# Optimization experiments

Measured on AMD Instinct MI355X. Metric: run time of the kernel, lower is better.

The kernel has to match this reference:

```python
import math
import jax, jax.numpy as jnp
from jax import lax
import numpy as np

C_CURV = 0.01
CHUNK = 1024
EPS = 1e-15
TANH_CLIP = 1.0 - 1e-6


def safe_norm(x):
    return jnp.maximum(jnp.linalg.norm(x, axis=-1, keepdims=True), EPS)


def exp_map_zero(v, c):
    sqrt_c = math.sqrt(c)
    vn = safe_norm(v)
    return jnp.tanh(sqrt_c * vn) * v / (sqrt_c * vn)


def log_map_zero(y, c):
    sqrt_c = math.sqrt(c)
    yn = safe_norm(y)
    arg = jnp.clip(sqrt_c * yn, -TANH_CLIP, TANH_CLIP)
    return jnp.arctanh(arg) * y / (sqrt_c * yn)


def mobius_add(x, y, c):
    x2 = jnp.sum(x * x, axis=-1, keepdims=True)
    y2 = jnp.sum(y * y, axis=-1, keepdims=True)
    xy = jnp.sum(x * y, axis=-1, keepdims=True)
    num = (1.0 + 2.0 * c * xy + c * y2) * x + (1.0 - c * x2) * y
    den = 1.0 + 2.0 * c * xy + (c * c) * x2 * y2
    return num / jnp.maximum(den, EPS)


def givens_rotation(x, angles):
    # x: (B, d), angles: (B, d/2)
    x1 = x[:, 0::2]
    x2 = x[:, 1::2]
    cos_a = jnp.cos(angles)
    sin_a = jnp.sin(angles)
    out1 = cos_a * x1 - sin_a * x2
    out2 = sin_a * x1 + cos_a * x2
    # interleave back: stack on axis 2 then flatten
    return jnp.stack([out1, out2], axis=2).reshape(x.shape[0], x.shape[1])


def setup_inputs() -> dict:
    key = jax.random.key(0)
    k1, k2, k3, k4, k5, k6 = jax.random.split(key, 6)
    E, R, D, B = 40960, 480, 512, 128
    # keep entity points well inside the Poincare ball of curvature c
    entity_embedding = 0.05 * jax.random.normal(k1, (E, D), dtype=jnp.float32)
    rel_embedding = jax.random.normal(k2, (R, D), dtype=jnp.float32)  # unused, interface parity
    rel_rot = jax.random.uniform(k3, (R, D // 2), dtype=jnp.float32,
                                 minval=-math.pi, maxval=math.pi)
    rel_trans = jax.random.uniform(k4, (R, D), dtype=jnp.float32,
                                   minval=-0.001, maxval=0.001)
    entity_bias = jnp.zeros((E,), dtype=jnp.float32)
    triplets = jax.random.randint(k6, (B, 3), 0, R, dtype=jnp.int64)
    return {
        "entity_embedding": entity_embedding,
        "rel_embedding": rel_embedding,
        "rel_rot": rel_rot,
        "rel_trans": rel_trans,
        "entity_bias": entity_bias,
        "triplets": triplets,
    }


def reference(entity_embedding, rel_embedding, rel_rot, rel_trans, entity_bias, triplets):
    c = C_CURV
    E, D = entity_embedding.shape
    r_idx = triplets[:, 1]
    s_emb = entity_embedding[triplets[:, 0]]            # (B, d)
    s_tan = log_map_zero(s_emb, c)
    rot_s_tan = givens_rotation(s_tan, rel_rot[r_idx])
    rot_s = exp_map_zero(rot_s_tan, c)
    t_r = exp_map_zero(rel_trans[r_idx], c)
    query = mobius_add(rot_s, t_r, c)                   # (B, d)

    n_chunks = E // CHUNK
    ent_chunks = entity_embedding.reshape(n_chunks, CHUNK, D)
    bias_chunks = entity_bias.reshape(n_chunks, CHUNK)

    neg_q = -query[:, None, :]                          # (B, 1, d)

    def body(_, inp):
        cand, b = inp                                   # (CHUNK, d), (CHUNK,)
        diff = mobius_add(neg_q, cand[None, :, :], c)   # (B, CHUNK, d)
        dist_sq = jnp.sum(diff * diff, axis=-1)         # (B, CHUNK)
        return None, -dist_sq + b[None, :]

    _, chunks = lax.scan(body, None, (ent_chunks, bias_chunks))  # (n_chunks, B, CHUNK)
    scores = jnp.transpose(chunks, (1, 0, 2)).reshape(query.shape[0], E)
    scores = scores + entity_bias[triplets[:, 0]][:, None]
    return scores
```

## Files before the change

kernel.cpp:

```cpp
#include <hip/hip_runtime.h>
#include <math.h>

#define C_C   0.01f
#define SQC   0.1f
#define EPSF  1e-15f
#define TCLIP (1.0f - 1e-6f)

typedef short short8 __attribute__((ext_vector_type(8)));
typedef float f32x4  __attribute__((ext_vector_type(4)));

__device__ __forceinline__ float wred(float v) {
#pragma unroll
    for (int off = 32; off > 0; off >>= 1) v += __shfl_xor(v, off, 64);
    return v;
}

__device__ __forceinline__ float dot4(const float4& a, const float4& b) {
    return a.x * b.x + a.y * b.y + a.z * b.z + a.w * b.w;
}

__device__ __forceinline__ unsigned int f2bf(float f) {
    unsigned int u = __float_as_uint(f);
    u += 0x7fffu + ((u >> 16) & 1u);
    return u >> 16;
}
__device__ __forceinline__ unsigned int pk2(float a, float b) {
    return f2bf(a) | (f2bf(b) << 16);
}

__global__ __launch_bounds__(64)
void build_queries(const float* __restrict__ ent,
                   const float* __restrict__ rrot,
                   const float* __restrict__ rtrans,
                   const float* __restrict__ ebias,
                   const int* __restrict__ trip,
                   unsigned short* __restrict__ qb,
                   float* __restrict__ q2buf,
                   float* __restrict__ sbbuf)
{
    const int b    = blockIdx.x;
    const int lane = threadIdx.x;
    const int t0   = trip[b * 3 + 0];
    const int r    = trip[b * 3 + 1];

    const float* srow = ent + (size_t)t0 * 512;
    float4 s0 = *(const float4*)(srow + 4 * lane);
    float4 s1 = *(const float4*)(srow + 256 + 4 * lane);

    float ss = dot4(s0, s0) + dot4(s1, s1);
    ss = wred(ss);
    float yn  = fmaxf(sqrtf(ss), EPSF);
    float arg = fminf(SQC * yn, TCLIP);
    float fl  = atanhf(arg) / (SQC * yn);

    const float* arow = rrot + (size_t)r * 256;
    float2 a01 = *(const float2*)(arow + 2 * lane);
    float2 a23 = *(const float2*)(arow + 128 + 2 * lane);
    float c0, n0, c1, n1, c2, n2, c3, n3;
    sincosf(a01.x, &n0, &c0);
    sincosf(a01.y, &n1, &c1);
    sincosf(a23.x, &n2, &c2);
    sincosf(a23.y, &n3, &c3);

    float t0x = s0.x * fl, t0y = s0.y * fl, t0z = s0.z * fl, t0w = s0.w * fl;
    float t1x = s1.x * fl, t1y = s1.y * fl, t1z = s1.z * fl, t1w = s1.w * fl;

    float4 r0, r1;
    r0.x = c0 * t0x - n0 * t0y;  r0.y = n0 * t0x + c0 * t0y;
    r0.z = c1 * t0z - n1 * t0w;  r0.w = n1 * t0z + c1 * t0w;
    r1.x = c2 * t1x - n2 * t1y;  r1.y = n2 * t1x + c2 * t1y;
    r1.z = c3 * t1z - n3 * t1w;  r1.w = n3 * t1z + c3 * t1w;

    float vv = dot4(r0, r0) + dot4(r1, r1);
    vv = wred(vv);
    float vn = fmaxf(sqrtf(vv), EPSF);
    float fx = tanhf(SQC * vn) / (SQC * vn);

    const float* trow = rtrans + (size_t)r * 512;
    float4 u0 = *(const float4*)(trow + 4 * lane);
    float4 u1 = *(const float4*)(trow + 256 + 4 * lane);
    float tt = dot4(u0, u0) + dot4(u1, u1);
    float rt = dot4(r0, u0) + dot4(r1, u1);
    tt = wred(tt);
    rt = wred(rt);
    float tn = fmaxf(sqrtf(tt), EPSF);
    float fy = tanhf(SQC * tn) / (SQC * tn);

    float x2 = fx * fx * vv;
    float y2 = fy * fy * tt;
    float xy = fx * fy * rt;
    float ca  = 1.0f + 2.0f * C_C * xy + C_C * y2;
    float cb  = 1.0f - C_C * x2;
    float den = fmaxf(1.0f + 2.0f * C_C * xy + C_C * C_C * x2 * y2, EPSF);
    float inv = 1.0f / den;

    float4 q0, q1;
    q0.x = (ca * fx * r0.x + cb * fy * u0.x) * inv;
    q0.y = (ca * fx * r0.y + cb * fy * u0.y) * inv;
    q0.z = (ca * fx * r0.z + cb * fy * u0.z) * inv;
    q0.w = (ca * fx * r0.w + cb * fy * u0.w) * inv;
    q1.x = (ca * fx * r1.x + cb * fy * u1.x) * inv;
    q1.y = (ca * fx * r1.y + cb * fy * u1.y) * inv;
    q1.z = (ca * fx * r1.z + cb * fy * u1.z) * inv;
    q1.w = (ca * fx * r1.w + cb * fy * u1.w) * inv;

    float qq = dot4(q0, q0) + dot4(q1, q1);
    qq = wred(qq);

    unsigned short* qrow = qb + (size_t)b * 512;
    uint2 h0, h1;
    h0.x = pk2(q0.x, q0.y);  h0.y = pk2(q0.z, q0.w);
    h1.x = pk2(q1.x, q1.y);  h1.y = pk2(q1.z, q1.w);
    *(uint2*)(qrow + 4 * lane)       = h0;
    *(uint2*)(qrow + 256 + 4 * lane) = h1;
    if (lane == 0) {
        q2buf[b] = qq;
        sbbuf[b] = ebias[t0];
    }
}

__global__ __launch_bounds__(64, 4)
void score_direct(const float* __restrict__ ent,
                  const float* __restrict__ ebias,
                  const unsigned short* __restrict__ qb,
                  const float* __restrict__ q2buf,
                  const float* __restrict__ sbbuf,
                  float* __restrict__ out, int E)
{
    const int lane = threadIdx.x;
    const int er   = lane & 15;
    const int kg   = lane >> 4;
    const int e0   = blockIdx.x * 16;

    short8 eb[16];
    float  e2p = 0.0f;
    const float* esrc = ent + (size_t)(e0 + er) * 512 + kg * 8;
#pragma unroll
    for (int ks = 0; ks < 16; ++ks) {
        float4 f0 = *(const float4*)(esrc + ks * 32);
        float4 f1 = *(const float4*)(esrc + ks * 32 + 4);
        e2p += dot4(f0, f0) + dot4(f1, f1);
        uint4 p = { pk2(f0.x, f0.y), pk2(f0.z, f0.w),
                    pk2(f1.x, f1.y), pk2(f1.z, f1.w) };
        eb[ks] = *(short8*)&p;
    }
    e2p += __shfl_xor(e2p, 16, 64);
    e2p += __shfl_xor(e2p, 32, 64);
    const float e2 = e2p;
    const float be = ebias[e0 + er];

    for (int qg = 0; qg < 8; ++qg) {
        f32x4 acc = (f32x4)0.0f;
        const unsigned short* qp =
            qb + (size_t)(qg * 16 + er) * 512 + kg * 8;
#pragma unroll
        for (int ks = 0; ks < 16; ++ks) {
            short8 a = *(const short8*)(qp + ks * 32);
            acc = __builtin_amdgcn_mfma_f32_16x16x32_bf16(a, eb[ks], acc,
                                                          0, 0, 0);
        }
        float4 q2v = *(const float4*)(q2buf + qg * 16 + kg * 4);
        float4 sbv = *(const float4*)(sbbuf + qg * 16 + kg * 4);
        const float q2a[4] = { q2v.x, q2v.y, q2v.z, q2v.w };
        const float sba[4] = { sbv.x, sbv.y, sbv.z, sbv.w };
#pragma unroll
        for (int r = 0; r < 4; ++r) {
            const int q   = qg * 16 + kg * 4 + r;
            float q2  = q2a[r];
            float xy  = -acc[r];
            float ca  = 1.0f + 2.0f * C_C * xy + C_C * e2;
            float cb  = 1.0f - C_C * q2;
            float den = fmaxf(1.0f + 2.0f * C_C * xy + C_C * C_C * q2 * e2, EPSF);
            float id2 = 1.0f / (den * den);
            float dist = (ca * ca * q2 + 2.0f * ca * cb * xy + cb * cb * e2) * id2;
            out[(size_t)q * E + e0 + er] = sba[r] + be - dist;
        }
    }
}

extern "C" void kernel_launch(void* const* d_in, const int* in_sizes, int n_in,
                              void* d_out, int out_size, void* d_ws, size_t ws_size,
                              hipStream_t stream) {
    const float* ent    = (const float*)d_in[0];
    const float* rrot   = (const float*)d_in[2];
    const float* rtrans = (const float*)d_in[3];
    const float* ebias  = (const float*)d_in[4];
    const int*   trip   = (const int*)d_in[5];
    float* out = (float*)d_out;

    const int B = in_sizes[5] / 3;
    const int E = in_sizes[0] / 512;

    unsigned short* qb = (unsigned short*)d_ws;
    float* q2buf = (float*)(qb + (size_t)B * 512);
    float* sbbuf = q2buf + B;

    build_queries<<<B, 64, 0, stream>>>(ent, rrot, rtrans, ebias, trip,
                                        qb, q2buf, sbbuf);
    score_direct<<<E / 16, 64, 0, stream>>>(ent, ebias, qb, q2buf, sbbuf,
                                            out, E);
}
```

Before: 171.4 us.

## Split K dimension across four waves with LDS reduction in scoring kernel

The scoring kernel now uses 256-thread blocks where each of four wavefronts handles a 128-wide slice of the 512-dim reduction for the same 16 entities. Partial MFMA accumulators are reduced through shared memory in two steps, and each wave then finishes the distance epilogue for two query groups. It also software-prefetches the next query group's bf16 fragments while issuing MFMAs. This aims to expose more parallelism and cut the per-wave serial MFMA chain and register footprint, at the cost of LDS traffic and two block barriers.

New measurement: 170.1 us. No clear change (-0.8%).

```diff
diff --git a/kernel.cpp b/kernel.cpp
--- a/kernel.cpp
+++ b/kernel.cpp
@@ -119,26 +119,36 @@
     }
 }
 
-__global__ __launch_bounds__(64, 4)
-void score_direct(const float* __restrict__ ent,
+__global__ __launch_bounds__(256, 4)
+void score_ksplit(const float* __restrict__ ent,
                   const float* __restrict__ ebias,
                   const unsigned short* __restrict__ qb,
                   const float* __restrict__ q2buf,
                   const float* __restrict__ sbbuf,
                   float* __restrict__ out, int E)
 {
-    const int lane = threadIdx.x;
+    __shared__ float part[2][8][64][4];
+    __shared__ float e2part[4][16];
+
+    const int tid  = threadIdx.x;
+    const int lane = tid & 63;
+    const int w    = tid >> 6;
     const int er   = lane & 15;
     const int kg   = lane >> 4;
     const int e0   = blockIdx.x * 16;
-
-    short8 eb[16];
+    const int k0   = w * 128 + kg * 8;
+
+    const float* esrc = ent + (size_t)(e0 + er) * 512 + k0;
+    float4 f[8];
+#pragma unroll
+    for (int i = 0; i < 8; ++i)
+        f[i] = *(const float4*)(esrc + (i >> 1) * 32 + (i & 1) * 4);
+
+    short8 eb[4];
     float  e2p = 0.0f;
-    const float* esrc = ent + (size_t)(e0 + er) * 512 + kg * 8;
-#pragma unroll
-    for (int ks = 0; ks < 16; ++ks) {
-        float4 f0 = *(const float4*)(esrc + ks * 32);
-        float4 f1 = *(const float4*)(esrc + ks * 32 + 4);
+#pragma unroll
+    for (int ks = 0; ks < 4; ++ks) {
+        float4 f0 = f[2 * ks], f1 = f[2 * ks + 1];
         e2p += dot4(f0, f0) + dot4(f1, f1);
         uint4 p = { pk2(f0.x, f0.y), pk2(f0.z, f0.w),
                     pk2(f1.x, f1.y), pk2(f1.z, f1.w) };
@@ -146,28 +156,69 @@
     }
     e2p += __shfl_xor(e2p, 16, 64);
     e2p += __shfl_xor(e2p, 32, 64);
-    const float e2 = e2p;
+    if (lane < 16) e2part[w][er] = e2p;
+
+    const unsigned short* qbase = qb + (size_t)er * 512 + k0;
+    f32x4 acc[8];
+#pragma unroll
+    for (int qg = 0; qg < 8; ++qg) acc[qg] = (f32x4)0.0f;
+
+    short8 qa[4], qn[4];
+#pragma unroll
+    for (int ks = 0; ks < 4; ++ks)
+        qa[ks] = *(const short8*)(qbase + ks * 32);
+
+#pragma unroll
+    for (int qg = 0; qg < 8; ++qg) {
+        if (qg < 7) {
+#pragma unroll
+            for (int ks = 0; ks < 4; ++ks)
+                qn[ks] = *(const short8*)(qbase + (size_t)(qg + 1) * 16 * 512
+                                          + ks * 32);
+        }
+#pragma unroll
+        for (int ks = 0; ks < 4; ++ks)
+            acc[qg] = __builtin_amdgcn_mfma_f32_16x16x32_bf16(
+                qa[ks], eb[ks], acc[qg], 0, 0, 0);
+#pragma unroll
+        for (int ks = 0; ks < 4; ++ks) qa[ks] = qn[ks];
+    }
+
+    if (w < 2) {
+#pragma unroll
+        for (int qg = 0; qg < 8; ++qg)
+            *(f32x4*)&part[w][qg][lane][0] = acc[qg];
+    }
+    __syncthreads();
+    if (w >= 2) {
+#pragma unroll
+        for (int qg = 0; qg < 8; ++qg) {
+            f32x4 v = *(f32x4*)&part[w - 2][qg][lane][0];
+            v += acc[qg];
+            *(f32x4*)&part[w - 2][qg][lane][0] = v;
+        }
+    }
+    __syncthreads();
+
+    const float e2 = e2part[0][er] + e2part[1][er] +
+                     e2part[2][er] + e2part[3][er];
     const float be = ebias[e0 + er];
-
-    for (int qg = 0; qg < 8; ++qg) {
-        f32x4 acc = (f32x4)0.0f;
-        const unsigned short* qp =
-            qb + (size_t)(qg * 16 + er) * 512 + kg * 8;
-#pragma unroll
-        for (int ks = 0; ks < 16; ++ks) {
-            short8 a = *(const short8*)(qp + ks * 32);
-            acc = __builtin_amdgcn_mfma_f32_16x16x32_bf16(a, eb[ks], acc,
-                                                          0, 0, 0);
-        }
+#pragma unroll
+    for (int i = 0; i < 2; ++i) {
+        const int qg = w * 2 + i;
+        f32x4 d0 = *(f32x4*)&part[0][qg][lane][0];
+        f32x4 d1 = *(f32x4*)&part[1][qg][lane][0];
+        f32x4 d  = d0 + d1;
+
         float4 q2v = *(const float4*)(q2buf + qg * 16 + kg * 4);
         float4 sbv = *(const float4*)(sbbuf + qg * 16 + kg * 4);
         const float q2a[4] = { q2v.x, q2v.y, q2v.z, q2v.w };
         const float sba[4] = { sbv.x, sbv.y, sbv.z, sbv.w };
 #pragma unroll
         for (int r = 0; r < 4; ++r) {
-            const int q   = qg * 16 + kg * 4 + r;
+            const int q  = qg * 16 + kg * 4 + r;
             float q2  = q2a[r];
-            float xy  = -acc[r];
+            float xy  = -d[r];
             float ca  = 1.0f + 2.0f * C_C * xy + C_C * e2;
             float cb  = 1.0f - C_C * q2;
             float den = fmaxf(1.0f + 2.0f * C_C * xy + C_C * C_C * q2 * e2, EPSF);
@@ -197,6 +248,6 @@
 
     build_queries<<<B, 64, 0, stream>>>(ent, rrot, rtrans, ebias, trip,
                                         qb, q2buf, sbbuf);
-    score_direct<<<E / 16, 64, 0, stream>>>(ent, ebias, qb, q2buf, sbbuf,
-                                            out, E);
-}
+    score_ksplit<<<E / 16, 256, 0, stream>>>(ent, ebias, qb, q2buf, sbbuf,
+                                             out, E);
+}
```
